# Optimization experiments

Hardware: AMD Instinct MI355X
Metric: run time of the kernel (lower is better)

Reference implementation:

```python
import jax, jax.numpy as jnp
import numpy as np

# --- static config matching init_kwargs ---
L = 6            # discretization level -> 2^L Euler substeps per unit time
T = 10           # number of time units
N = 1000         # number of particles
DX = 16          # state dim (== obs dim)
INIT_VAL = 0.0
SUB = 2 ** L
HL = 2.0 ** (-L)
S = SUB * T + 1  # total path length


def setup_inputs() -> dict:
    key = jax.random.key(0)
    k1, k2, k3, k4 = jax.random.split(key, 4)
    input_path = jax.random.normal(k1, (S, DX), dtype=jnp.float32) * 0.1
    observe_path = jax.random.normal(k2, (T + 1, DX), dtype=jnp.float32) * 0.5
    # stable linear drift mu(x) = x @ A.T, constant diffusion matrix Sig
    A = (-0.5 * jnp.eye(DX) + 0.05 * jax.random.normal(k3, (DX, DX))).astype(jnp.float32)
    Sig = (0.3 * jnp.eye(DX) + 0.02 * jax.random.normal(k4, (DX, DX))).astype(jnp.float32)
    return {"input_path": input_path, "observe_path": observe_path, "A": A, "Sig": Sig}


def _mu(x, A):
    return x @ A.T


def _llg(x, y):
    # Gaussian observation log-likelihood per particle: x (N,DX), y (DX,)
    return -0.5 * jnp.sum((y - x) ** 2, axis=-1)


def _euler_segment(x0, A, Sig, key):
    # unit_path_update: 2^L Euler-Maruyama steps; returns (SUB, N, DX)
    dw = jax.random.normal(key, (SUB, x0.shape[0], DX)) * np.sqrt(HL).astype(np.float32)
    def step(x, d):
        xn = x + _mu(x, A) * HL + d @ Sig.T
        return xn, xn
    _, seg = jax.lax.scan(step, x0, dw)
    return seg


def _multinomial_idx(wn, dice):
    bins = jnp.cumsum(wn)
    bins = bins.at[-1].set(jnp.maximum(1.0, bins[-1]))  # bins[-1] = max(1, bins[-1])
    return jnp.clip(jnp.searchsorted(bins, dice, side="right"), 0, N - 1)


def _forward(input_path, observe_path, A, Sig):
    key = jax.random.key(42)
    un = jnp.full((S, N, DX), INIT_VAL, dtype=input_path.dtype)
    un_hat = jnp.full((S, N, DX), INIT_VAL, dtype=input_path.dtype)
    gn = jnp.zeros((N,), dtype=input_path.dtype)
    wn = jnp.full((N,), 1.0 / N, dtype=input_path.dtype)
    for t in range(T):  # static unroll over time units (indices are static)
        start, upd = SUB * t, SUB * (t + 1)
        kdw = jax.random.fold_in(key, 2 * t)
        kres = jax.random.fold_in(key, 2 * t + 1)
        un = un.at[: start + 1].set(un_hat[: start + 1])
        seg = _euler_segment(un[start], A, Sig, kdw)
        un = un.at[start + 1 : upd + 1].set(seg)
        un = un.at[:, -1, :].set(input_path)  # pin conditioned path as last particle
        gn = _llg(un[upd], observe_path[t + 1]) + gn
        wn = jax.nn.softmax(gn)  # exp(gn - max)/sum, numerically stable
        ess = 1.0 / jnp.sum(wn ** 2)
        do_rs = ess <= N / 2
        idx = _multinomial_idx(wn, jax.random.uniform(kres, (N,)))
        prefix = un[: upd + 1]
        gathered = prefix[:, idx, :]
        new_prefix = jnp.where(do_rs, gathered, prefix)
        gn = jnp.where(do_rs, jnp.zeros_like(gn), gn)
        un_hat = un_hat.at[: upd + 1].set(new_prefix)
        un_hat = un_hat.at[:, -1, :].set(input_path)
    # sample_output: draw one particle index from final weights
    kfin = jax.random.fold_in(key, 2 * T)
    i0 = _multinomial_idx(wn, jax.random.uniform(kfin, (1,)))[0]
    return un[:, i0, :]  # (S, DX)


def reference(input_path, observe_path, A, Sig):
    return _forward(input_path, observe_path, A, Sig)
```

## Files before the change

kernel.cpp:

```cpp
#include <hip/hip_runtime.h>
#include <cstdint>
#include <cstddef>

#pragma clang fp contract(off)


typedef unsigned int u32;

#define NP   1000
#define DXC  16
#define SUBC 64
#define TC   10
#define SC   641

#define WS_XS   0
#define WS_ANC  160000
#define WS_XF0  170032
#define WS_XF1  186032
#define WS_GN0  202032
#define WS_GN1  203032
#define WS_LG0  204032
#define WS_LG1  205032
#define WS_DSG  206032

__device__ __forceinline__ u32 rotl32(u32 v, u32 d) { return (v << d) | (v >> (32u - d)); }

__device__ __forceinline__ void tf2x32(u32 k0, u32 k1, u32 c0, u32 c1, u32& o0, u32& o1) {
  u32 ks0 = k0, ks1 = k1, ks2 = k0 ^ k1 ^ 0x1BD11BDAu;
  u32 x0 = c0 + ks0, x1 = c1 + ks1;
  x0 += x1; x1 = rotl32(x1,13); x1 ^= x0;
  x0 += x1; x1 = rotl32(x1,15); x1 ^= x0;
  x0 += x1; x1 = rotl32(x1,26); x1 ^= x0;
  x0 += x1; x1 = rotl32(x1, 6); x1 ^= x0;
  x0 += ks1; x1 += ks2 + 1u;
  x0 += x1; x1 = rotl32(x1,17); x1 ^= x0;
  x0 += x1; x1 = rotl32(x1,29); x1 ^= x0;
  x0 += x1; x1 = rotl32(x1,16); x1 ^= x0;
  x0 += x1; x1 = rotl32(x1,24); x1 ^= x0;
  x0 += ks2; x1 += ks0 + 2u;
  x0 += x1; x1 = rotl32(x1,13); x1 ^= x0;
  x0 += x1; x1 = rotl32(x1,15); x1 ^= x0;
  x0 += x1; x1 = rotl32(x1,26); x1 ^= x0;
  x0 += x1; x1 = rotl32(x1, 6); x1 ^= x0;
  x0 += ks0; x1 += ks1 + 3u;
  x0 += x1; x1 = rotl32(x1,17); x1 ^= x0;
  x0 += x1; x1 = rotl32(x1,29); x1 ^= x0;
  x0 += x1; x1 = rotl32(x1,16); x1 ^= x0;
  x0 += x1; x1 = rotl32(x1,24); x1 ^= x0;
  x0 += ks1; x1 += ks2 + 4u;
  x0 += x1; x1 = rotl32(x1,13); x1 ^= x0;
  x0 += x1; x1 = rotl32(x1,15); x1 ^= x0;
  x0 += x1; x1 = rotl32(x1,26); x1 ^= x0;
  x0 += x1; x1 = rotl32(x1, 6); x1 ^= x0;
  x0 += ks2; x1 += ks0 + 5u;
  o0 = x0; o1 = x1;
}

__device__ __forceinline__ u32 bits32p(u32 k0, u32 k1, u32 i) {
  u32 o0, o1; tf2x32(k0, k1, 0u, i, o0, o1); return o0 ^ o1;
}

__device__ __forceinline__ float u01(u32 b) {
  return __uint_as_float((b >> 9) | 0x3f800000u) - 1.0f;
}

__device__ __forceinline__ float xla_exp(float input) {
#pragma clang fp contract(off)
  float x = fminf(input, 88.3762626647950f);
  x = fmaxf(x, -88.3762626647949f);
  float fx = floorf(__builtin_fmaf(x, 1.44269504088896341f, 0.5f));
  float tmp = 0.693359375f * fx;
  float z0  = -2.12194440e-4f * fx;
  float xr = x - tmp;
  xr = xr - z0;
  float z = xr * xr;
  float y = __builtin_fmaf(xr, 1.9875691500e-4f, 1.3981999507e-3f);
  y = __builtin_fmaf(y, xr, 8.3334519073e-3f);
  y = __builtin_fmaf(y, xr, 4.1665795894e-2f);
  y = __builtin_fmaf(y, xr, 1.6666665459e-1f);
  y = __builtin_fmaf(y, xr, 5.0000001201e-1f);
  y = __builtin_fmaf(y, z, xr);
  y = 1.0f + y;
  int n = (int)fx;
  float p2n = __uint_as_float((u32)(n + 127) << 23);
  float res = y * p2n;
  return fmaxf(res, input);
}

__device__ __forceinline__ float xla_log(float input) {
#pragma clang fp contract(off)
  float t0 = fmaxf(input, __uint_as_float(0x00800000u));
  u32 bi = __float_as_uint(t0);
  float e = (float)(int)((bi >> 23) - 126u);
  float x = __uint_as_float((bi & 0x807fffffu) | 0x3f000000u);
  float mo, mx;
  if (x < 0.707106781186547524f) { mx = x; mo = 1.0f; } else { mx = 0.0f; mo = 0.0f; }
  x = x - 1.0f;
  e = e - mo;
  x = x + mx;
  float z = x * x;
  float y = __builtin_fmaf(x, 7.0376836292e-2f, -1.1514610310e-1f);
  y = __builtin_fmaf(y, x, 1.1676998740e-1f);
  y = __builtin_fmaf(y, x, -1.2420140846e-1f);
  y = __builtin_fmaf(y, x, 1.4249322787e-1f);
  y = __builtin_fmaf(y, x, -1.6668057665e-1f);
  y = __builtin_fmaf(y, x, 2.0000714765e-1f);
  y = __builtin_fmaf(y, x, -2.4999993993e-1f);
  y = __builtin_fmaf(y, x, 3.3333331174e-1f);
  y = y * x;
  y = y * z;
  y = __builtin_fmaf(e, -2.12194440e-4f, y);
  y = y - 0.5f * z;
  x = x + y;
  x = __builtin_fmaf(e, 0.693359375f, x);
  return x;
}

__device__ __forceinline__ float xla_log1p(float x) {
#pragma clang fp contract(off)
  float ax = fabsf(x);
  if (ax < 1e-4f) {
    float t = (-0.5f * x) + 1.0f;
    return t * x;
  }
  return xla_log(x + 1.0f);
}

__device__ __forceinline__ float xla_erfinv(float u) {
#pragma clang fp contract(off)
  float w = -xla_log1p((-u) * u);
  float p;
  if (w < 5.0f) {
    float ww = w - 2.5f;
    p = 2.81022636e-08f;
    p = 3.43273939e-07f  + p * ww;
    p = -3.5233877e-06f  + p * ww;
    p = -4.39150654e-06f + p * ww;
    p = 0.00021858087f   + p * ww;
    p = -0.00125372503f  + p * ww;
    p = -0.00417768164f  + p * ww;
    p = 0.246640727f     + p * ww;
    p = 1.50140941f      + p * ww;
  } else {
    float ww = (float)__builtin_sqrt((double)w) - 3.0f;
    p = -0.000200214257f;
    p = 0.000100950558f + p * ww;
    p = 0.00134934322f  + p * ww;
    p = -0.00367342844f + p * ww;
    p = 0.00573950773f  + p * ww;
    p = -0.0076224613f  + p * ww;
    p = 0.00943887047f  + p * ww;
    p = 1.00167406f     + p * ww;
    p = 2.83297682f     + p * ww;
  }
  return p * u;
}

#define U_LO __uint_as_float(0xBF7FFFFFu)

__device__ __forceinline__ float nrm(u32 bits) {
#pragma clang fp contract(off)
  float f = u01(bits);
  float u = (f * 2.0f) + U_LO;
  u = fmaxf(U_LO, u);
  return __uint_as_float(0x3FB504F3u) * xla_erfinv(u);
}

__device__ __forceinline__ void gen_vals(int t, int blk, int tid,
                                         const float* __restrict__ Sg_s,
                                         float* __restrict__ dg) {
#pragma clang fp contract(off)
  int nl = tid & 7;
  int s  = tid >> 3;
  int n  = blk * 8 + nl;
  u32 k0, k1; tf2x32(0u, 42u, 0u, (u32)(2 * t), k0, k1);
  float dwv[DXC];
#pragma unroll
  for (int k = 0; k < DXC; ++k) {
    u32 b = bits32p(k0, k1, (u32)(s * 16000 + n * 16 + k));
    dwv[k] = nrm(b) * 0.125f;
  }
#pragma unroll
  for (int d = 0; d < DXC; ++d) {
    float g = 0.0f;
#pragma unroll
    for (int k = 0; k < DXC; ++k) g = __builtin_fmaf(dwv[k], Sg_s[d * 16 + k], g);
    dg[d] = g;
  }
}

__device__ __forceinline__ void gen_unit(int t, int blk, int tid,
                                         const float* __restrict__ Sg_s,
                                         float* __restrict__ wsf) {
  float dg[DXC];
  gen_vals(t, blk, tid, Sg_s, dg);
  int gtid = (t * 125 + blk) * 512 + tid;
  float* dst = wsf + WS_DSG + (size_t)gtid * 16;
#pragma unroll
  for (int d = 0; d < DXC; ++d) dst[d] = dg[d];
}

__device__ void cumsum_tree_par(const float* x0, float* out0, float* scr, int tid) {
#pragma clang fp contract(off)
  const int nlv[10] = {1000, 500, 250, 125, 62, 31, 15, 7, 3, 1};
  const float* raw[10]; float* scn[10]; float* rawm[10];
  raw[0] = x0; scn[0] = out0;
  int off = 0;
  for (int k = 1; k < 10; ++k) {
    rawm[k] = scr + off; raw[k] = rawm[k]; off += nlv[k];
    scn[k] = scr + off; off += nlv[k];
  }
  for (int k = 0; k < 9; ++k) {
    int nr = nlv[k + 1];
    for (int i = tid; i < nr; i += 512) rawm[k + 1][i] = raw[k][2 * i] + raw[k][2 * i + 1];
    __syncthreads();
  }
  if (tid == 0) scn[9][0] = raw[9][0];
  __syncthreads();
  for (int k = 8; k >= 0; --k) {
    int nk = nlv[k], nr = nlv[k + 1];
    if (tid == 0) scn[k][0] = raw[k][0];
    for (int i = tid; i < nr; i += 512) scn[k][2 * i + 1] = scn[k + 1][i];
    if ((nk & 1) == 0) {
      for (int i = 1 + tid; i < nr; i += 512) scn[k][2 * i] = scn[k + 1][i - 1] + raw[k][2 * i];
    } else {
      for (int i = 1 + tid; i <= nr; i += 512) scn[k][2 * i] = scn[k + 1][i - 1] + raw[k][2 * i];
    }
    __syncthreads();
  }
}

__device__ void filter_step(int s, float* __restrict__ wsf, int tid, int wr,
                            float* gn_s, float* e_s, float* wn_s, float* bins_s,
                            float* scr_s, float* red_s, int* src_s) {
#pragma clang fp contract(off)
  const float* LLGp = wsf + ((s & 1) ? WS_LG1 : WS_LG0);
  const float* GNp = wsf + (((s & 1) ^ 1) ? WS_GN1 : WS_GN0);
  float* GNw = wsf + ((s & 1) ? WS_GN1 : WS_GN0);
  int* ANC = (int*)(wsf + WS_ANC);

  for (int n = tid; n < NP; n += 512) {
    float l = LLGp[n];
    float gp = (s == 0) ? 0.0f : GNp[n];
    gn_s[n] = l + gp;
  }
  __syncthreads();
  {
    float mv = -__builtin_inff();
    for (int n = tid; n < NP; n += 512) mv = fmaxf(mv, gn_s[n]);
#pragma unroll
    for (int off = 32; off >= 1; off >>= 1) mv = fmaxf(mv, __shfl_xor(mv, off));
    if ((tid & 63) == 0) red_s[tid >> 6] = mv;
  }
  __syncthreads();
  float m;
  {
    float a = fmaxf(fmaxf(red_s[0], red_s[1]), fmaxf(red_s[2], red_s[3]));
    float b = fmaxf(fmaxf(red_s[4], red_s[5]), fmaxf(red_s[6], red_s[7]));
    m = fmaxf(a, b);
  }
  for (int n = tid; n < NP; n += 512) e_s[n] = xla_exp(gn_s[n] - m);
  __syncthreads();
  if (tid < 8) {
    float a = 0.0f;
    for (int c = 0; c < 5; ++c) {
      float v[25];
#pragma unroll
      for (int j = 0; j < 25; ++j) v[j] = e_s[(c * 25 + j) * 8 + tid];
#pragma unroll
      for (int j = 0; j < 25; ++j) a = a + v[j];
    }
    red_s[tid] = a;
  }
  __syncthreads();
  float ssum;
  {
    float b0 = red_s[0] + red_s[4], b1 = red_s[1] + red_s[5],
          b2 = red_s[2] + red_s[6], b3 = red_s[3] + red_s[7];
    float c0 = b0 + b2, c1 = b1 + b3;
    ssum = c0 + c1;
  }
  for (int n = tid; n < NP; n += 512) wn_s[n] = e_s[n] / ssum;
  __syncthreads();
  if (tid < 8) {
    float a = 0.0f;
    for (int c = 0; c < 5; ++c) {
      float v[25];
#pragma unroll
      for (int j = 0; j < 25; ++j) v[j] = wn_s[(c * 25 + j) * 8 + tid];
#pragma unroll
      for (int j = 0; j < 25; ++j) { float q = v[j] * v[j]; a = a + q; }
    }
    red_s[tid] = a;
  }
  __syncthreads();
  int rs;
  {
    float b0 = red_s[0] + red_s[4], b1 = red_s[1] + red_s[5],
          b2 = red_s[2] + red_s[6], b3 = red_s[3] + red_s[7];
    float c0 = b0 + b2, c1 = b1 + b3;
    float ss = c0 + c1;
    float ess = 1.0f / ss;
    rs = (ess <= 500.0f) ? 1 : 0;
  }
  cumsum_tree_par(wn_s, bins_s, scr_s, tid);
  if (tid == 0) bins_s[NP - 1] = fmaxf(1.0f, bins_s[NP - 1]);
  __syncthreads();
  u32 kr0, kr1; tf2x32(0u, 42u, 0u, (u32)(2 * s + 1), kr0, kr1);
  for (int n = tid; n < NP; n += 512) {
    u32 b = bits32p(kr0, kr1, (u32)n);
    float dice = fmaxf(0.0f, u01(b));
    int lo = 0, hi = NP;
    while (lo < hi) { int mid = (lo + hi) >> 1; if (bins_s[mid] <= dice) lo = mid + 1; else hi = mid; }
    int idx = lo > NP - 1 ? NP - 1 : lo;
    int a = rs ? idx : n;
    src_s[n] = (n == NP - 1) ? (NP - 1) : a;
    if (wr) {
      ANC[s * NP + n] = a;
      GNw[n] = rs ? 0.0f : gn_s[n];
    }
  }
  __syncthreads();
}

__global__ __launch_bounds__(512, 1) void k_step(const float* __restrict__ inp,
                                                 const float* __restrict__ obs,
                                                 const float* __restrict__ A,
                                                 const float* __restrict__ Sg,
                                                 float* __restrict__ wsf, int t) {
#pragma clang fp contract(off)
  __shared__ float Sg_s[256];
  __shared__ float dsg_s[8192];
  __shared__ float gn_s[NP], e_s[NP], wn_s[NP], bins_s[NP], scr_s[2048];
  __shared__ float red_s[8];
  __shared__ int src_s[NP];
  int tid = threadIdx.x;
  int bid = (int)blockIdx.x;
  if (bid >= 125) {
    if (t + 1 < TC) {
      if (tid < 256) Sg_s[tid] = Sg[tid];
      __syncthreads();
      gen_unit(t + 1, bid - 125, tid, Sg_s, wsf);
    }
    return;
  }
  int base = bid * 8;
  if (t == 0) {
    if (tid < 256) Sg_s[tid] = Sg[tid];
    __syncthreads();
    float dg[DXC];
    gen_vals(0, bid, tid, Sg_s, dg);
    float* dst = wsf + WS_DSG + ((size_t)bid * 512 + tid) * 16;
#pragma unroll
    for (int d = 0; d < DXC; ++d) {
      dst[d] = dg[d];
      dsg_s[tid * 16 + d] = dg[d];
    }
    __syncthreads();
  } else {
    float r[16];
    const float* DSG = wsf + WS_DSG + (size_t)t * 1024000 + (size_t)bid * 8192;
#pragma unroll
    for (int j = 0; j < 16; ++j) r[j] = DSG[j * 512 + tid];
    filter_step(t - 1, wsf, tid, bid == 0,
                gn_s, e_s, wn_s, bins_s, scr_s, red_s, src_s);
#pragma unroll
    for (int j = 0; j < 16; ++j) dsg_s[j * 512 + tid] = r[j];
    __syncthreads();
  }
  if (tid < 128) {
    int p = tid >> 4, d = tid & 15;
    int n = base + p;
    float Ar[DXC];
#pragma unroll
    for (int k = 0; k < DXC; ++k) Ar[k] = A[d * 16 + k];
    float x = 0.0f;
    if (t > 0) {
      const float* XFp = wsf + (((t - 1) & 1) ? WS_XF1 : WS_XF0);
      int s0 = src_s[n];
      x = (s0 == NP - 1) ? inp[(SUBC * t) * 16 + d] : XFp[s0 * 16 + d];
    }
    wsf[WS_XS + t * 16000 + n * 16 + d] = x;
    for (int sl = 0; sl < SUBC; ++sl) {
      float mu = 0.0f;
#pragma unroll
      for (int k = 0; k < DXC; ++k) {
        float xk = __shfl(x, k, 16);
        mu = __builtin_fmaf(xk, Ar[k], mu);
      }
      float t2 = x + mu * 0.015625f;
      x = t2 + dsg_s[sl * 128 + p * 16 + d];
    }
    float* XFc = wsf + ((t & 1) ? WS_XF1 : WS_XF0);
    XFc[n * 16 + d] = x;
    int upd = SUBC * (t + 1);
    float fv = (n == NP - 1) ? inp[upd * 16 + d] : x;
    float dd = obs[(t + 1) * 16 + d] - fv;
    float sacc = 0.0f;
#pragma unroll
    for (int k = 0; k < DXC; ++k) {
      float v = __shfl(dd, k, 16);
      float sq = v * v;
      sacc = sacc + sq;
    }
    if (d == 0) {
      float* LLGw = wsf + ((t & 1) ? WS_LG1 : WS_LG0);
      LLGw[n] = -0.5f * sacc;
    }
  }
}

__global__ __launch_bounds__(512, 1) void k_out(const float* __restrict__ inp,
                                                const float* __restrict__ A,
                                                float* __restrict__ wsf,
                                                float* __restrict__ out) {
#pragma clang fp contract(off)
  __shared__ float gn_s[NP], e_s[NP], wn_s[NP], bins_s[NP], scr_s[2048];
  __shared__ float red_s[8];
  __shared__ int src_s[NP];
  __shared__ float dsg_t[1024];
  __shared__ int lin_s[24];
  int tid = threadIdx.x;
  int bid = (int)blockIdx.x;
  filter_step(TC - 1, wsf, tid, 0,
              gn_s, e_s, wn_s, bins_s, scr_s, red_s, src_s);
  if (tid == 0) {
    const int* ANC = (const int*)(wsf + WS_ANC);
    u32 kf0, kf1; tf2x32(0u, 42u, 0u, (u32)(2 * TC), kf0, kf1);
    u32 b = bits32p(kf0, kf1, 0u);
    float dice = fmaxf(0.0f, u01(b));
    int lo = 0, hi = NP;
    while (lo < hi) { int mid = (lo + hi) >> 1; if (bins_s[mid] <= dice) lo = mid + 1; else hi = mid; }
    int i0 = lo > NP - 1 ? NP - 1 : lo;
    lin_s[0] = i0;
    lin_s[1 + 9] = i0;
    int hit = (i0 == NP - 1) ? 1 : 0;
    lin_s[11 + 9] = hit;
    int j = i0;
    for (int u = 8; u >= 0; --u) {
      j = ANC[u * NP + j];
      if (j == NP - 1) hit = 1;
      lin_s[1 + u] = j;
      lin_s[11 + u] = hit;
    }
  }
  __syncthreads();
  int i0 = lin_s[0];
  int i = bid * 512 + tid;
  if (i < SC * DXC) {
    int srow = i >> 4;
    if (i0 == NP - 1) out[i] = inp[i];
    else if (srow == 0) out[i] = lin_s[11 + 0] ? inp[i] : 0.0f;
    else { int u = (srow - 1) >> 6; if (lin_s[11 + u]) out[i] = inp[i]; }
  }
  if (bid >= TC) return;
  if (i0 == NP - 1) return;
  int u = bid;
  if (lin_s[11 + u]) return;
  int p = lin_s[1 + u];
  const float* DSG = wsf + WS_DSG + (size_t)u * 1024000 + (size_t)(p >> 3) * 8192
                     + (size_t)(p & 7) * 16;
  {
    int idx = tid;
    int sl = idx >> 4, d = idx & 15;
    dsg_t[idx] = DSG[sl * 128 + d];
    idx = 512 + tid;
    sl = idx >> 4; d = idx & 15;
    dsg_t[idx] = DSG[sl * 128 + d];
  }
  __syncthreads();
  if (tid < 16) {
    int d = tid;
    float Ar[DXC];
#pragma unroll
    for (int k = 0; k < DXC; ++k) Ar[k] = A[d * 16 + k];
    float x = wsf[WS_XS + u * 16000 + p * 16 + d];
    for (int sl = 0; sl < SUBC; ++sl) {
      float mu = 0.0f;
#pragma unroll
      for (int k = 0; k < DXC; ++k) {
        float xk = __shfl(x, k, 16);
        mu = __builtin_fmaf(xk, Ar[k], mu);
      }
      float t2 = x + mu * 0.015625f;
      x = t2 + dsg_t[sl * 16 + d];
      out[(u * SUBC + sl + 1) * DXC + d] = x;
    }
  }
}

extern "C" void kernel_launch(void* const* d_in, const int* in_sizes, int n_in,
                              void* d_out, int out_size, void* d_ws, size_t ws_size,
                              hipStream_t stream) {
  (void)in_sizes; (void)n_in; (void)out_size; (void)ws_size;
  const float* inp = (const float*)d_in[0];
  const float* obs = (const float*)d_in[1];
  const float* A   = (const float*)d_in[2];
  const float* Sg  = (const float*)d_in[3];
  float* wsf = (float*)d_ws;
  float* out = (float*)d_out;

  for (int t = 0; t < TC; ++t) {
    k_step<<<dim3(250), dim3(512), 0, stream>>>(inp, obs, A, Sg, wsf, t);
  }
  k_out<<<dim3(21), dim3(512), 0, stream>>>(inp, A, wsf, out);
}
```

Measured before the change: 305.5 us.

## Run weight normalisation and cumsum in one wavefront, resample only block's particles

The normalisation, ESS and prefix-sum tree move into a single 64-lane wavefront that uses volatile shared memory instead of block-wide barriers, removing roughly twenty __syncthreads per filter step. Non-leader blocks now binary-search only the 8 particles they own rather than all 1000; block 0 still computes everything and writes ancestors and gn. The cumsum now runs on 64 threads instead of 512, which lengthens the serial work, and it relies on implicit wavefront lockstep for correctness.

Result: slower. 357.2 us (+16.9%).

```diff
diff --git a/kernel.cpp b/kernel.cpp
--- a/kernel.cpp
+++ b/kernel.cpp
@@ -200,37 +200,48 @@
   for (int d = 0; d < DXC; ++d) dst[d] = dg[d];
 }
 
-__device__ void cumsum_tree_par(const float* x0, float* out0, float* scr, int tid) {
+__device__ void cumsum_wave_vol(volatile float* x0, volatile float* out0,
+                                volatile float* scr, int lane) {
 #pragma clang fp contract(off)
   const int nlv[10] = {1000, 500, 250, 125, 62, 31, 15, 7, 3, 1};
-  const float* raw[10]; float* scn[10]; float* rawm[10];
+  volatile float* raw[10]; volatile float* scn[10];
   raw[0] = x0; scn[0] = out0;
   int off = 0;
   for (int k = 1; k < 10; ++k) {
-    rawm[k] = scr + off; raw[k] = rawm[k]; off += nlv[k];
+    raw[k] = scr + off; off += nlv[k];
     scn[k] = scr + off; off += nlv[k];
   }
   for (int k = 0; k < 9; ++k) {
     int nr = nlv[k + 1];
-    for (int i = tid; i < nr; i += 512) rawm[k + 1][i] = raw[k][2 * i] + raw[k][2 * i + 1];
-    __syncthreads();
-  }
-  if (tid == 0) scn[9][0] = raw[9][0];
-  __syncthreads();
+    for (int i = lane; i < nr; i += 64) {
+      float a = raw[k][2 * i];
+      float b = raw[k][2 * i + 1];
+      raw[k + 1][i] = a + b;
+    }
+  }
+  if (lane == 0) scn[9][0] = raw[9][0];
   for (int k = 8; k >= 0; --k) {
     int nk = nlv[k], nr = nlv[k + 1];
-    if (tid == 0) scn[k][0] = raw[k][0];
-    for (int i = tid; i < nr; i += 512) scn[k][2 * i + 1] = scn[k + 1][i];
+    if (lane == 0) scn[k][0] = raw[k][0];
+    for (int i = lane; i < nr; i += 64) scn[k][2 * i + 1] = scn[k + 1][i];
     if ((nk & 1) == 0) {
-      for (int i = 1 + tid; i < nr; i += 512) scn[k][2 * i] = scn[k + 1][i - 1] + raw[k][2 * i];
+      for (int i = 1 + lane; i < nr; i += 64) {
+        float a = scn[k + 1][i - 1];
+        float b = raw[k][2 * i];
+        scn[k][2 * i] = a + b;
+      }
     } else {
-      for (int i = 1 + tid; i <= nr; i += 512) scn[k][2 * i] = scn[k + 1][i - 1] + raw[k][2 * i];
-    }
-    __syncthreads();
-  }
-}
-
-__device__ void filter_step(int s, float* __restrict__ wsf, int tid, int wr,
+      for (int i = 1 + lane; i <= nr; i += 64) {
+        float a = scn[k + 1][i - 1];
+        float b = raw[k][2 * i];
+        scn[k][2 * i] = a + b;
+      }
+    }
+  }
+}
+
+__device__ void filter_step(int s, float* __restrict__ wsf, int tid,
+                            int src_mode, int base,
                             float* gn_s, float* e_s, float* wn_s, float* bins_s,
                             float* scr_s, float* red_s, int* src_s) {
 #pragma clang fp contract(off)
@@ -261,63 +272,81 @@
   }
   for (int n = tid; n < NP; n += 512) e_s[n] = xla_exp(gn_s[n] - m);
   __syncthreads();
-  if (tid < 8) {
-    float a = 0.0f;
-    for (int c = 0; c < 5; ++c) {
-      float v[25];
-#pragma unroll
-      for (int j = 0; j < 25; ++j) v[j] = e_s[(c * 25 + j) * 8 + tid];
-#pragma unroll
-      for (int j = 0; j < 25; ++j) a = a + v[j];
-    }
-    red_s[tid] = a;
-  }
-  __syncthreads();
-  float ssum;
-  {
-    float b0 = red_s[0] + red_s[4], b1 = red_s[1] + red_s[5],
-          b2 = red_s[2] + red_s[6], b3 = red_s[3] + red_s[7];
-    float c0 = b0 + b2, c1 = b1 + b3;
-    ssum = c0 + c1;
-  }
-  for (int n = tid; n < NP; n += 512) wn_s[n] = e_s[n] / ssum;
-  __syncthreads();
-  if (tid < 8) {
-    float a = 0.0f;
-    for (int c = 0; c < 5; ++c) {
-      float v[25];
-#pragma unroll
-      for (int j = 0; j < 25; ++j) v[j] = wn_s[(c * 25 + j) * 8 + tid];
-#pragma unroll
-      for (int j = 0; j < 25; ++j) { float q = v[j] * v[j]; a = a + q; }
-    }
-    red_s[tid] = a;
-  }
-  __syncthreads();
-  int rs;
-  {
-    float b0 = red_s[0] + red_s[4], b1 = red_s[1] + red_s[5],
-          b2 = red_s[2] + red_s[6], b3 = red_s[3] + red_s[7];
-    float c0 = b0 + b2, c1 = b1 + b3;
-    float ss = c0 + c1;
-    float ess = 1.0f / ss;
-    rs = (ess <= 500.0f) ? 1 : 0;
-  }
-  cumsum_tree_par(wn_s, bins_s, scr_s, tid);
-  if (tid == 0) bins_s[NP - 1] = fmaxf(1.0f, bins_s[NP - 1]);
-  __syncthreads();
+  if (tid < 64) {
+    volatile float* vred = red_s;
+    volatile float* vwn  = wn_s;
+    volatile float* vbin = bins_s;
+    volatile float* vscr = scr_s;
+    if (tid < 8) {
+      float a = 0.0f;
+      for (int c = 0; c < 5; ++c) {
+        float v[25];
+#pragma unroll
+        for (int j = 0; j < 25; ++j) v[j] = e_s[(c * 25 + j) * 8 + tid];
+#pragma unroll
+        for (int j = 0; j < 25; ++j) a = a + v[j];
+      }
+      vred[tid] = a;
+    }
+    float ssum;
+    {
+      float r0 = vred[0], r1 = vred[1], r2 = vred[2], r3 = vred[3];
+      float r4 = vred[4], r5 = vred[5], r6 = vred[6], r7 = vred[7];
+      float b0 = r0 + r4, b1 = r1 + r5, b2 = r2 + r6, b3 = r3 + r7;
+      float c0 = b0 + b2, c1 = b1 + b3;
+      ssum = c0 + c1;
+    }
+    for (int i = tid; i < NP; i += 64) vwn[i] = e_s[i] / ssum;
+    if (tid < 8) {
+      float a = 0.0f;
+      for (int c = 0; c < 5; ++c) {
+        float v[25];
+#pragma unroll
+        for (int j = 0; j < 25; ++j) v[j] = vwn[(c * 25 + j) * 8 + tid];
+#pragma unroll
+        for (int j = 0; j < 25; ++j) { float q = v[j] * v[j]; a = a + q; }
+      }
+      vred[tid] = a;
+    }
+    int rs;
+    {
+      float r0 = vred[0], r1 = vred[1], r2 = vred[2], r3 = vred[3];
+      float r4 = vred[4], r5 = vred[5], r6 = vred[6], r7 = vred[7];
+      float b0 = r0 + r4, b1 = r1 + r5, b2 = r2 + r6, b3 = r3 + r7;
+      float c0 = b0 + b2, c1 = b1 + b3;
+      float ss = c0 + c1;
+      float ess = 1.0f / ss;
+      rs = (ess <= 500.0f) ? 1 : 0;
+    }
+    if (tid == 0) vred[0] = rs ? 1.0f : 0.0f;
+    cumsum_wave_vol(vwn, vbin, vscr, tid);
+    if (tid == 0) vbin[NP - 1] = fmaxf(1.0f, vbin[NP - 1]);
+  }
+  __syncthreads();
+  int rs = (red_s[0] != 0.0f);
   u32 kr0, kr1; tf2x32(0u, 42u, 0u, (u32)(2 * s + 1), kr0, kr1);
-  for (int n = tid; n < NP; n += 512) {
-    u32 b = bits32p(kr0, kr1, (u32)n);
-    float dice = fmaxf(0.0f, u01(b));
-    int lo = 0, hi = NP;
-    while (lo < hi) { int mid = (lo + hi) >> 1; if (bins_s[mid] <= dice) lo = mid + 1; else hi = mid; }
-    int idx = lo > NP - 1 ? NP - 1 : lo;
-    int a = rs ? idx : n;
-    src_s[n] = (n == NP - 1) ? (NP - 1) : a;
-    if (wr) {
+  if (src_mode == 2) {
+    for (int n = tid; n < NP; n += 512) {
+      u32 b = bits32p(kr0, kr1, (u32)n);
+      float dice = fmaxf(0.0f, u01(b));
+      int lo = 0, hi = NP;
+      while (lo < hi) { int mid = (lo + hi) >> 1; if (bins_s[mid] <= dice) lo = mid + 1; else hi = mid; }
+      int idx = lo > NP - 1 ? NP - 1 : lo;
+      int a = rs ? idx : n;
+      src_s[n] = (n == NP - 1) ? (NP - 1) : a;
       ANC[s * NP + n] = a;
       GNw[n] = rs ? 0.0f : gn_s[n];
+    }
+  } else if (src_mode == 1) {
+    if (tid < 8) {
+      int n = base + tid;
+      u32 b = bits32p(kr0, kr1, (u32)n);
+      float dice = fmaxf(0.0f, u01(b));
+      int lo = 0, hi = NP;
+      while (lo < hi) { int mid = (lo + hi) >> 1; if (bins_s[mid] <= dice) lo = mid + 1; else hi = mid; }
+      int idx = lo > NP - 1 ? NP - 1 : lo;
+      int a = rs ? idx : n;
+      src_s[n] = (n == NP - 1) ? (NP - 1) : a;
     }
   }
   __syncthreads();
@@ -362,7 +391,7 @@
     const float* DSG = wsf + WS_DSG + (size_t)t * 1024000 + (size_t)bid * 8192;
 #pragma unroll
     for (int j = 0; j < 16; ++j) r[j] = DSG[j * 512 + tid];
-    filter_step(t - 1, wsf, tid, bid == 0,
+    filter_step(t - 1, wsf, tid, (bid == 0) ? 2 : 1, base,
                 gn_s, e_s, wn_s, bins_s, scr_s, red_s, src_s);
 #pragma unroll
     for (int j = 0; j < 16; ++j) dsg_s[j * 512 + tid] = r[j];
@@ -422,7 +451,7 @@
   __shared__ int lin_s[24];
   int tid = threadIdx.x;
   int bid = (int)blockIdx.x;
-  filter_step(TC - 1, wsf, tid, 0,
+  filter_step(TC - 1, wsf, tid, 0, 0,
               gn_s, e_s, wn_s, bins_s, scr_s, red_s, src_s);
   if (tid == 0) {
     const int* ANC = (const int*)(wsf + WS_ANC);
```
